# Performance work log

Measured on AMD Instinct MI355X. Metric: run time of the kernel, lower is better.

Reference implementation:

```python
import jax, jax.numpy as jnp
import numpy as np

B, TD, TC = 64, 800, 80
ENC, H, MA, MO = 128, 400, 10, 20
OUT = MO * 6 + 1  # 121


def _lstm(x, h0, c0, Wih, Whh, bih, bhh):
    # x: (B,T,I); PyTorch gate order i,f,g,o
    xg = jnp.einsum('bti,gi->btg', x, Wih) + (bih + bhh)  # (B,T,4H)
    def step(carry, xg_t):
        h, c = carry
        g = xg_t + h @ Whh.T
        i, f, gg, o = jnp.split(g, 4, axis=-1)
        c = jax.nn.sigmoid(f) * c + jax.nn.sigmoid(i) * jnp.tanh(gg)
        h = jax.nn.sigmoid(o) * jnp.tanh(c)
        return (h, c), h
    (_, _), hs = jax.lax.scan(step, (h0, c0), xg.transpose(1, 0, 2))
    return hs.transpose(1, 0, 2)  # (B,T,H)


def setup_inputs() -> dict:
    key = jax.random.key(0)
    ks = jax.random.split(key, 16)
    s = 0.05
    rn = lambda k, sh, sc=1.0: jax.random.normal(k, sh, jnp.float32) * sc
    I1 = 3 + ENC + H
    return {
        'strokes': rn(ks[0], (B, TD, 3)),
        'context': rn(ks[1], (B, TC, ENC)),
        'context_mask': jnp.ones((B, TC), jnp.float32),
        'h_0': rn(ks[2], (3, 2 * H), s),
        'Wih0': rn(ks[3], (4 * H, 3), s), 'Whh0': rn(ks[4], (4 * H, H), s),
        'bih0': jnp.zeros((4 * H,), jnp.float32), 'bhh0': jnp.zeros((4 * H,), jnp.float32),
        'Wih1': rn(ks[5], (4 * H, I1), s), 'Whh1': rn(ks[6], (4 * H, H), s),
        'bih1': jnp.zeros((4 * H,), jnp.float32), 'bhh1': jnp.zeros((4 * H,), jnp.float32),
        'Wih2': rn(ks[7], (4 * H, I1), s), 'Whh2': rn(ks[8], (4 * H, H), s),
        'bih2': jnp.zeros((4 * H,), jnp.float32), 'bhh2': jnp.zeros((4 * H,), jnp.float32),
        'attn_W': rn(ks[9], (3 * MA, H), s), 'attn_b': jnp.zeros((3 * MA,), jnp.float32),
        'out_W': rn(ks[10], (OUT, 3 * H), s), 'out_b': jnp.zeros((OUT,), jnp.float32),
    }


def reference(strokes, context, context_mask, h_0,
              Wih0, Whh0, bih0, bhh0,
              Wih1, Whh1, bih1, bhh1,
              Wih2, Whh2, bih2, bhh2,
              attn_W, attn_b, out_W, out_b):
    bsz = strokes.shape[0]
    # initial states: h_0[l] split into (h, c)
    init = [(jnp.broadcast_to(h_0[l, :H], (bsz, H)), jnp.broadcast_to(h_0[l, H:], (bsz, H))) for l in range(3)]

    h0s = _lstm(strokes, init[0][0], init[0][1], Wih0, Whh0, bih0, bhh0)  # (B,TD,H)

    # Gaussian monotonic attention
    p = jnp.exp(h0s @ attn_W.T + attn_b)  # (B,TD,3MA)
    alpha, beta, kappa = jnp.split(p, 3, axis=-1)
    kappa = jnp.cumsum(0.2 * kappa, axis=1)  # (B,TD,MA)
    u = jnp.arange(TC, dtype=jnp.float32)  # (TC,)
    # phi: (B,TD,TC)
    diff = kappa[:, :, None, :] - u[None, None, :, None]
    phi = jnp.sum(alpha[:, :, None, :] * jnp.exp(-beta[:, :, None, :] * diff * diff), axis=-1)
    w = jnp.einsum('btu,bue->bte', phi * context_mask[:, None, :], context)  # (B,TD,ENC)

    x1 = jnp.concatenate([strokes, h0s, w], axis=2)
    h1s = _lstm(x1, init[1][0], init[1][1], Wih1, Whh1, bih1, bhh1)
    x2 = jnp.concatenate([strokes, h1s, w], axis=2)
    h2s = _lstm(x2, init[2][0], init[2][1], Wih2, Whh2, bih2, bhh2)

    outputs = jnp.concatenate([h0s, h1s, h2s], axis=-1) @ out_W.T + out_b  # (B,TD,121)
    return outputs
```

## Files before the change

### kernel.cpp

```cpp
#include <hip/hip_runtime.h>
#include <stdint.h>

typedef unsigned short u16;
typedef __attribute__((ext_vector_type(8))) short bf16x8;
typedef __attribute__((ext_vector_type(4))) float f32x4;
typedef __attribute__((ext_vector_type(4))) int   i32x4;
typedef __attribute__((ext_vector_type(4))) unsigned short u16x4;

#define DI static __device__ __forceinline__

constexpr int B_   = 64;
constexpr int TD   = 800;
constexpr int TC   = 80;
constexpr int ENC  = 128;
constexpr int H    = 400;
constexpr int OUTN = 121;

constexpr int HP   = 416;
constexpr int KT_H = 13;
constexpr int KOP  = 1216;
constexpr int NOP  = 128;
constexpr int NBL  = 25;
constexpr int NBA  = 32;
constexpr int CSTR = 32;
constexpr int FSLOT= 32;

constexpr size_t HB_B  = (size_t)(TD+1)*B_*HP*2;
constexpr size_t WBF_B = (size_t)TD*B_*ENC*2;
constexpr size_t STR_B = (size_t)TD*B_*4*4;
constexpr size_t APK_B = (size_t)NBL*4*KT_H*64*8*2;
constexpr size_t WF_B  = (size_t)NBL*4*17*64*8*2;

constexpr size_t OFF_HB0 = 0;
constexpr size_t OFF_HB1 = OFF_HB0 + HB_B;
constexpr size_t OFF_HB2 = OFF_HB1 + HB_B;
constexpr size_t OFF_HLO = OFF_HB2 + HB_B;
constexpr size_t OFF_WBF = OFF_HLO + HB_B;
constexpr size_t OFF_STR = OFF_WBF + WBF_B;
constexpr size_t OFF_APKH= OFF_STR + STR_B;
constexpr size_t OFF_APKL= OFF_APKH + 3*APK_B;
constexpr size_t OFF_WF1 = OFF_APKL + APK_B;
constexpr size_t OFF_WF2 = OFF_WF1 + WF_B;
constexpr size_t OFF_OUW = OFF_WF2 + WF_B;
constexpr size_t OFF_BIA = OFF_OUW + (size_t)NOP*KOP*2;
constexpr size_t OFF_CNT = OFF_BIA + (size_t)3*1600*4;
constexpr size_t WS_NEED = OFF_CNT + (size_t)4*FSLOT*CSTR*4 + 256;

constexpr int LDS_DUMP = 0;
constexpr int LDS_CL   = 66560;
constexpr int LDS_EX   = 70656;
constexpr int LDS_W3   = 140288;
constexpr int LDS_BIAS = 141056;
constexpr int LDSB     = 141312;
constexpr int ALDS_CTX = 0;
constexpr int ALDS_ATW = 81920;
constexpr int ALDS_H   = 130040;
constexpr int ALDS_PHI = 133240;
constexpr int ALDS_MSK = 133880;
constexpr int ALDS_KAP = 134520;
constexpr int ALDS_P   = 134600;
constexpr int ALDS_PPS = 134840;

DI u16 f2b(float f){ union{float f; unsigned u;} v; v.f=f; unsigned r = v.u + 0x7FFFu + ((v.u>>16)&1u); return (u16)(r>>16); }
DI float b2f(u16 h){ union{unsigned u; float f;} v; v.u=((unsigned)h)<<16; return v.f; }
DI float sigm(float x){ return 1.f/(1.f+__expf(-x)); }
DI float tanh_(float x){ float a=fabsf(x), e=__expf(-2.f*a), t=(1.f-e)/(1.f+e); return x<0.f ? -t : t; }

DI void st16(u16* p, u16 v){
  asm volatile("global_store_short %0, %1, off sc0 sc1" :: "v"(p), "v"((unsigned)v) : "memory");
}
DI void st8(u16* p, u16x4 v){
  unsigned long long x; __builtin_memcpy(&x, &v, 8);
  asm volatile("global_store_dwordx2 %0, %1, off sc0 sc1" :: "v"(p), "v"(x) : "memory");
}
DI void setflag(unsigned* p, unsigned t){
  asm volatile("global_store_dword %0, %1, off sc0 sc1" :: "v"(p), "v"(t) : "memory");
}
DI void waitflags2(const unsigned* fA, int nA, unsigned tA,
                   const unsigned* fB, int nB, unsigned tB){
  int lane = threadIdx.x & 63;
  const unsigned* p; unsigned tgt;
  if (lane < nA)            { p = fA + (size_t)lane*CSTR;        tgt = tA; }
  else if (lane < nA+nB)    { p = fB + (size_t)(lane-nA)*CSTR;   tgt = tB; }
  else                      { p = fA;                            tgt = 0;  }
  while (1) {
    unsigned v = __hip_atomic_load(p, __ATOMIC_RELAXED, __HIP_MEMORY_SCOPE_AGENT);
    if (__all(v >= tgt)) break;
    __builtin_amdgcn_s_sleep(1);
  }
  asm volatile("" ::: "memory");
}

__global__ void k_init(const float* __restrict__ h0, u16* hb0, u16* hb1, u16* hb2, u16* hlo,
                       unsigned* cnt){
  int i = blockIdx.x*256 + threadIdx.x;
  const int nA = 3*B_*HP, nA2 = B_*HP, nB = 4*TD*B_*16, nC = 4*FSLOT;
  if (i < nA) {
    int l = i/(B_*HP); int rem = i - l*(B_*HP); int b = rem/HP; int k = rem - b*HP;
    u16 v = (k<H) ? f2b(h0[l*800 + k]) : (u16)0;
    (l==0?hb0:(l==1?hb1:hb2))[(size_t)b*HP + k] = v;
  } else if (i < nA+nA2) {
    int rem = i - nA; int b = rem/HP; int k = rem - b*HP;
    u16 v = 0;
    if (k < H) { float w = h0[k]; u16 hi = f2b(w); v = f2b(w - b2f(hi)); }
    hlo[(size_t)b*HP + k] = v;
  } else if (i < nA+nA2+nB) {
    int q = i - nA - nA2; int buf = q/(TD*B_*16); int r2 = q % (TD*B_*16);
    int t = r2/(B_*16) + 1; int r3 = r2 % (B_*16); int b = r3>>4; int kk = r3&15;
    u16* hb = (buf==0)?hb0:((buf==1)?hb1:((buf==2)?hb2:hlo));
    hb[((size_t)t*B_ + b)*HP + 400 + kk] = 0;
  } else if (i < nA+nA2+nB+nC) {
    int q = i - nA - nA2 - nB;
    cnt[(size_t)q*CSTR] = 0u;
  }
}

__global__ void k_apack(const float* W0, const float* W1, const float* W2,
                        u16* apkHi, u16* apkLo){
  int i = blockIdx.x*256 + threadIdx.x;
  const int total = 3*NBL*4*KT_H*64;
  if (i >= total) return;
  int lane = i & 63; int r = i >> 6;
  int kt = r % KT_H; r /= KT_H;
  int mt = r % 4;    r /= 4;
  int j  = r % NBL;  int lv = r / NBL;
  const float* W = (lv==0)?W0:((lv==1)?W1:W2);
  int row = mt*400 + j*16 + (lane & 15);
  int kbase = kt*32 + (lane>>4)*8;
  #pragma unroll
  for (int e=0;e<8;++e){
    int k = kbase+e;
    float w = (k<H) ? W[(size_t)row*H + k] : 0.f;
    u16 hi = f2b(w);
    apkHi[(size_t)i*8 + e] = hi;
    if (lv == 0) apkLo[(size_t)i*8 + e] = f2b(w - b2f(hi));
  }
}

__global__ void k_wihpack2(const float* __restrict__ W, u16* __restrict__ dst){
  int i = blockIdx.x*256 + threadIdx.x;
  if (i >= NBL*4*17*64) return;
  int lane = i & 63; int r = i >> 6;
  int ktf = r % 17; r /= 17; int mt = r % 4; int j = r / 4;
  int row = mt*400 + j*16 + (lane & 15);
  int kbase = ktf*32 + (lane>>4)*8;
  #pragma unroll
  for (int e=0;e<8;++e){
    int k = kbase+e;
    int col;
    if (ktf < 13) col = (k < 400) ? (3 + k) : -1;
    else          col = 403 + (k - 416);
    dst[(size_t)i*8 + e] = (col >= 0) ? f2b(W[(size_t)row*531 + col]) : (u16)0;
  }
}

__global__ void k_smallpack(const float* outW,
                            const float* bi0, const float* bh0, const float* bi1, const float* bh1,
                            const float* bi2, const float* bh2,
                            u16* ouw, float* biasP){
  int i = blockIdx.x*256 + threadIdx.x;
  const int n2 = NOP*KOP, n3 = 3*1600;
  if (i < n2) {
    int n = i/KOP, k = i - n*KOP;
    ouw[i] = (n<OUTN && k<1200) ? f2b(outW[(size_t)n*1200 + k]) : (u16)0;
  } else if (i < n2+n3) {
    int q = i-n2; int l = q/1600, row = q - l*1600;
    const float* bi = (l==0)?bi0:((l==1)?bi1:bi2);
    const float* bh = (l==0)?bh0:((l==1)?bh1:bh2);
    biasP[q] = bi[row] + bh[row];
  }
}

__global__ void k_packs(const float* __restrict__ strokes, float* __restrict__ st){
  int i = blockIdx.x*256 + threadIdx.x;
  if (i >= TD*B_) return;
  int t = i / B_, b = i & 63;
  st[(size_t)i*4+0] = strokes[((size_t)b*TD + t)*3 + 0];
  st[(size_t)i*4+1] = strokes[((size_t)b*TD + t)*3 + 1];
  st[(size_t)i*4+2] = strokes[((size_t)b*TD + t)*3 + 2];
  st[(size_t)i*4+3] = 0.f;
}

template<int L>
DI void stage_lstm(char* smem, int j,
    const u16* __restrict__ apkHi,
    const u16* __restrict__ exG,
    const float* __restrict__ strokesT,
    const float* __restrict__ wihRaw, int wihStride,
    const float* __restrict__ biasL,
    const float* __restrict__ h0g,
    u16* __restrict__ hb_self, const u16* __restrict__ hb_prev,
    u16* __restrict__ hlo_, const u16* __restrict__ wbf,
    unsigned* __restrict__ fSelf, const unsigned* __restrict__ fDep, int nDep)
{
  float* dumpS = (float*)(smem + LDS_DUMP);
  float* cL    = (float*)(smem + LDS_CL);
  u16*   exS   = (u16*)  (smem + LDS_EX);
  float* w3S   = (float*)(smem + LDS_W3);
  float* biasS = (float*)(smem + LDS_BIAS);
  const int tid = threadIdx.x, wv = tid>>6, l = tid&63;
  const int col = l&15, kg = l>>4;

  bf16x8 ahi[4][4];
  #pragma unroll
  for (int mt=0;mt<4;++mt)
    #pragma unroll
    for (int i=0;i<4;++i){
      int kt = wv + i*4;
      if (kt < KT_H) ahi[mt][i] = *(const bf16x8*)(apkHi + (size_t)j*26624 + ((size_t)(mt*KT_H + kt)*64 + l)*8);
      else { bf16x8 z = {0,0,0,0,0,0,0,0}; ahi[mt][i] = z; }
    }
  {
    const int nv = (L==0) ? 3328 : 4352;
    const size_t stride = (L==0) ? 26624 : 34816;
    const i32x4* src = (const i32x4*)(exG + (size_t)j*stride);
    i32x4* dst = (i32x4*)exS;
    for (int i = tid; i < nv; i += 256) dst[i] = src[i];
  }
  if (tid < 192) {
    int local = tid/3, c = tid - (tid/3)*3;
    int row = (local>>4)*400 + j*16 + (local&15);
    w3S[tid] = wihRaw[(size_t)row*wihStride + c];
  }
  if (tid < 64) {
    int row = (tid>>4)*400 + j*16 + (tid&15);
    biasS[tid] = biasL[row];
  }
  for (int i = tid; i < 1024; i += 256) cL[i] = h0g[L*800 + 400 + j*16 + (i>>6)];
  __syncthreads();

  for (int t = 1; t <= TD; ++t) {
    if constexpr (L > 0) waitflags2(fDep, nDep, (unsigned)t, fSelf, NBL, (unsigned)(t-1));
    else                 waitflags2(fSelf, NBL, (unsigned)(t-1), nullptr, 0, 0u);
    f32x4 acc[4][4];
    #pragma unroll
    for (int mt=0;mt<4;++mt)
      #pragma unroll
      for (int nt=0;nt<4;++nt){ f32x4 z = {0.f,0.f,0.f,0.f}; acc[mt][nt] = z; }

    const u16* hbase = hb_self + (size_t)(t-1)*B_*HP + kg*8;
    const u16* lbase = (L==0) ? (hlo_ + (size_t)(t-1)*B_*HP + kg*8) : nullptr;
    #pragma unroll
    for (int i=0;i<4;++i){
      int kt = wv + i*4;
      if (kt < KT_H) {
        bf16x8 bhi[4], blo[4];
        #pragma unroll
        for (int nt=0;nt<4;++nt){
          bhi[nt] = *(const bf16x8*)(hbase + (size_t)(nt*16+col)*HP + kt*32);
          if constexpr (L==0) blo[nt] = *(const bf16x8*)(lbase + (size_t)(nt*16+col)*HP + kt*32);
        }
        #pragma unroll
        for (int mt=0;mt<4;++mt){
          bf16x8 a = ahi[mt][i];
          #pragma unroll
          for (int nt=0;nt<4;++nt)
            acc[mt][nt] = __builtin_amdgcn_mfma_f32_16x16x32_bf16(a, bhi[nt], acc[mt][nt], 0,0,0);
          if constexpr (L==0) {
            bf16x8 al = *(const bf16x8*)(exS + ((size_t)(mt*KT_H + kt)*64 + l)*8);
            #pragma unroll
            for (int nt=0;nt<4;++nt){
              acc[mt][nt] = __builtin_amdgcn_mfma_f32_16x16x32_bf16(a,  blo[nt], acc[mt][nt], 0,0,0);
              acc[mt][nt] = __builtin_amdgcn_mfma_f32_16x16x32_bf16(al, bhi[nt], acc[mt][nt], 0,0,0);
            }
          }
        }
      }
    }
    if constexpr (L > 0) {
      const u16* pbase = hb_prev + (size_t)t*B_*HP + kg*8;
      const u16* wbase = wbf + ((size_t)(t-1)*B_)*ENC + kg*8;
      #pragma unroll
      for (int i=0;i<5;++i){
        int ktf = wv + i*4;
        if (ktf < 17) {
          bf16x8 bfr[4];
          if (ktf < 13) {
            #pragma unroll
            for (int nt=0;nt<4;++nt) bfr[nt] = *(const bf16x8*)(pbase + (size_t)(nt*16+col)*HP + ktf*32);
          } else {
            #pragma unroll
            for (int nt=0;nt<4;++nt) bfr[nt] = *(const bf16x8*)(wbase + (size_t)(nt*16+col)*ENC + (ktf-13)*32);
          }
          #pragma unroll
          for (int mt=0;mt<4;++mt){
            bf16x8 a = *(const bf16x8*)(exS + ((size_t)(mt*17 + ktf)*64 + l)*8);
            #pragma unroll
            for (int nt=0;nt<4;++nt)
              acc[mt][nt] = __builtin_amdgcn_mfma_f32_16x16x32_bf16(a, bfr[nt], acc[mt][nt], 0,0,0);
          }
        }
      }
    }
    #pragma unroll
    for (int mt=0;mt<4;++mt)
      #pragma unroll
      for (int nt=0;nt<4;++nt)
        #pragma unroll
        for (int r=0;r<4;++r)
          dumpS[wv*4160 + (mt*16 + kg*4 + r)*65 + nt*16 + col] = acc[mt][nt][r];
    __syncthreads();
    {
      const int bg = tid & 63, uq = tid >> 6;
      const float* sp = strokesT + ((size_t)(t-1)*B_ + bg)*4;
      float sx = sp[0], sy = sp[1], sz = sp[2];
      u16x4 hh4, ll4;
      #pragma unroll
      for (int e=0;e<4;++e){
        int u = uq*4 + e;
        int idx = u*64 + bg;
        float gv[4];
        #pragma unroll
        for (int g=0; g<4; ++g){
          int row = g*16 + u;
          float s = dumpS[row*65 + bg] + dumpS[4160 + row*65 + bg]
                  + dumpS[8320 + row*65 + bg] + dumpS[12480 + row*65 + bg];
          s += biasS[row] + w3S[row*3+0]*sx + w3S[row*3+1]*sy + w3S[row*3+2]*sz;
          gv[g] = s;
        }
        float co = cL[idx];
        float i_ = sigm(gv[0]), f_ = sigm(gv[1]), g_ = tanh_(gv[2]), o_ = sigm(gv[3]);
        float cn = f_*co + i_*g_;
        cL[idx] = cn;
        float hv = o_*tanh_(cn);
        u16 hh = f2b(hv);
        hh4[e] = hh;
        if constexpr (L==0) ll4[e] = f2b(hv - b2f(hh));
      }
      st8(hb_self + ((size_t)t*B_ + bg)*HP + j*16 + uq*4, hh4);
      if constexpr (L==0) st8(hlo_ + ((size_t)t*B_ + bg)*HP + j*16 + uq*4, ll4);
    }
    __syncthreads();
    if (tid == 0) setflag(fSelf + (size_t)j*CSTR, (unsigned)t);
  }
}

DI void stage_attn(char* smem, int j2,
    const float* __restrict__ ctx, const float* __restrict__ cmask,
    const float* __restrict__ attnW, const float* __restrict__ attnB,
    const u16* __restrict__ hb0, const u16* __restrict__ hlo_,
    u16* __restrict__ wbf,
    const unsigned* __restrict__ fA, unsigned* __restrict__ fB)
{
  float* ctxS = (float*)(smem + ALDS_CTX);
  float* atwS = (float*)(smem + ALDS_ATW);
  float* hS   = (float*)(smem + ALDS_H);
  float* phiS = (float*)(smem + ALDS_PHI);
  float* mskS = (float*)(smem + ALDS_MSK);
  float* kapS = (float*)(smem + ALDS_KAP);
  float* pS   = (float*)(smem + ALDS_P);
  float* ppsS = (float*)(smem + ALDS_PPS);
  const int tid = threadIdx.x;
  const int b0 = j2*2;
  for (int i = tid; i < 2*80*128; i += 256) {
    int bi = i/10240, rem = i%10240;
    ctxS[i] = ctx[(size_t)(b0+bi)*10240 + rem];
  }
  for (int i = tid; i < 30*400; i += 256) {
    int row = i/400, k = i - row*400;
    atwS[row*401 + k] = attnW[i];
  }
  for (int i = tid; i < 160; i += 256) {
    int bi = i/80, u = i - bi*80;
    mskS[i] = cmask[(b0+bi)*80 + u];
  }
  if (tid < 20) kapS[tid] = 0.f;
  float aB = (tid < 60) ? attnB[tid % 30] : 0.f;
  __syncthreads();

  for (int t = 1; t <= TD; ++t) {
    waitflags2(fA, NBL, (unsigned)t, nullptr, 0, 0u);
    if (tid < 200) {
      int bi = tid/100, k = (tid%100)*4;
      size_t off = ((size_t)t*B_ + (b0+bi))*HP + k;
      u16x4 hi4 = *(const u16x4*)(hb0 + off);
      u16x4 lo4 = *(const u16x4*)(hlo_ + off);
      #pragma unroll
      for (int e=0;e<4;++e) hS[bi*400 + k + e] = b2f(hi4[e]) + b2f(lo4[e]);
    }
    __syncthreads();
    if (tid < 240) {
      int bi = tid/120, r = tid - bi*120;
      int row = r>>2, seg = r&3;
      const float* ar = atwS + row*401 + seg*100;
      const float* hr = hS + bi*400 + seg*100;
      float a0=0,a1=0,a2=0,a3=0;
      #pragma unroll 4
      for (int k=0;k<100;k+=4){
        a0 += ar[k]*hr[k]; a1 += ar[k+1]*hr[k+1];
        a2 += ar[k+2]*hr[k+2]; a3 += ar[k+3]*hr[k+3];
      }
      ppsS[(bi*30+row)*4+seg] = a0+a1+a2+a3;
    }
    __syncthreads();
    if (tid < 60) {
      int bi = tid/30, row = tid - bi*30;
      const float* pp = ppsS + (bi*30+row)*4;
      pS[bi*30+row] = __expf(pp[0]+pp[1]+pp[2]+pp[3] + aB);
    }
    __syncthreads();
    if (tid < 20) {
      int bi = tid/10, m = tid - bi*10;
      kapS[tid] += 0.2f * pS[bi*30 + 20 + m];
    }
    __syncthreads();
    if (tid < 160) {
      int bi = tid/80; float u2 = (float)(tid - bi*80);
      const float* pb = pS + bi*30; const float* kb = kapS + bi*10;
      float a = 0.f;
      #pragma unroll
      for (int m=0;m<10;++m){ float d = kb[m]-u2; a += pb[m]*__expf(-pb[10+m]*d*d); }
      phiS[tid] = a * mskS[tid];
    }
    __syncthreads();
    {
      int bi = tid >> 7, e = tid & 127;
      const float* ph = phiS + bi*80;
      const float* cs = ctxS + (size_t)bi*10240 + e;
      float a = 0.f;
      for (int u = 0; u < TC; ++u) a += ph[u]*cs[u*128];
      st16(wbf + ((size_t)(t-1)*B_ + (b0+bi))*ENC + e, f2b(a));
    }
    __syncthreads();
    if (tid == 0) setflag(fB + (size_t)j2*CSTR, (unsigned)t);
  }
}

__global__ __launch_bounds__(256,1) void k_mega(
    const u16* apkH, const u16* apkL, const u16* wf1, const u16* wf2,
    const float* strokesT, const float* Wih0, const float* Wih1, const float* Wih2,
    const float* bia, const float* h0g,
    u16* hb0, u16* hb1, u16* hb2, u16* hlo, u16* wbf,
    const float* ctx, const float* cmask, const float* attnW, const float* attnB,
    unsigned* cnt)
{
  extern __shared__ char smem[];
  unsigned* fA = cnt;
  unsigned* fB = cnt + (size_t)FSLOT*CSTR;
  unsigned* fC = cnt + (size_t)2*FSLOT*CSTR;
  unsigned* fD = cnt + (size_t)3*FSLOT*CSTR;
  int j = blockIdx.x;
  if (j < NBL) {
    stage_lstm<0>(smem, j, apkH, apkL, strokesT, Wih0, 3, bia, h0g,
                  hb0, nullptr, hlo, nullptr, fA, nullptr, 0);
  } else if (j < NBL+NBA) {
    stage_attn(smem, j-NBL, ctx, cmask, attnW, attnB, hb0, hlo, wbf, fA, fB);
  } else if (j < 2*NBL+NBA) {
    stage_lstm<1>(smem, j-NBL-NBA, apkH + (size_t)1*NBL*26624, wf1, strokesT, Wih1, 531,
                  bia+1600, h0g, hb1, hb0, nullptr, wbf, fC, fB, NBA);
  } else {
    stage_lstm<2>(smem, j-2*NBL-NBA, apkH + (size_t)2*NBL*26624, wf2, strokesT, Wih2, 531,
                  bia+3200, h0g, hb2, hb1, nullptr, wbf, fD, fC, NBL);
  }
}

__global__ __launch_bounds__(256) void k_gemm_out(const u16* __restrict__ hb0, const u16* __restrict__ hb1,
                                                  const u16* __restrict__ hb2, const u16* __restrict__ ouw,
                                                  const float* __restrict__ out_b, float* __restrict__ dout){
  int wv = threadIdx.x>>6, l = threadIdx.x&63;
  int task = blockIdx.x*4 + wv;
  int ng = task & 1; int mpair = task >> 1;
  int m0 = mpair*32; int t = m0>>6; int broff = m0 & 63;
  int col = l&15, kg = l>>4;
  f32x4 acc[2][4];
  #pragma unroll
  for (int mt=0;mt<2;++mt)
    #pragma unroll
    for (int nt=0;nt<4;++nt){ f32x4 z = {0.f,0.f,0.f,0.f}; acc[mt][nt] = z; }
  for (int kt=0; kt<38; ++kt) {
    int k0 = kt*32 + kg*8;
    int reg = (k0>=800) ? 2 : ((k0>=400) ? 1 : 0);
    int koff = k0 - reg*400;
    const u16* hb = (reg==0) ? hb0 : ((reg==1) ? hb1 : hb2);
    bf16x8 afr[2];
    #pragma unroll
    for (int mt=0;mt<2;++mt)
      afr[mt] = *(const bf16x8*)(hb + ((size_t)(t+1)*B_ + broff + mt*16 + col)*HP + koff);
    #pragma unroll
    for (int nt=0;nt<4;++nt) {
      bf16x8 bfr = *(const bf16x8*)(ouw + (size_t)(ng*64 + nt*16 + col)*KOP + k0);
      #pragma unroll
      for (int mt=0;mt<2;++mt)
        acc[mt][nt] = __builtin_amdgcn_mfma_f32_16x16x32_bf16(afr[mt], bfr, acc[mt][nt], 0,0,0);
    }
  }
  #pragma unroll
  for (int mt=0;mt<2;++mt)
    #pragma unroll
    for (int nt=0;nt<4;++nt)
      #pragma unroll
      for (int r=0;r<4;++r) {
        int n = ng*64 + nt*16 + col;
        int bo = broff + mt*16 + kg*4 + r;
        if (n < OUTN) dout[((size_t)bo*TD + t)*OUTN + n] = acc[mt][nt][r] + out_b[n];
      }
}

__global__ void k_sentinel(float* o, float code){ o[threadIdx.x] = code; }

extern "C" void kernel_launch(void* const* d_in, const int* in_sizes, int n_in,
                              void* d_out, int out_size, void* d_ws, size_t ws_size,
                              hipStream_t stream) {
  const float* strokes = (const float*)d_in[0];
  const float* context = (const float*)d_in[1];
  const float* cmask   = (const float*)d_in[2];
  const float* h0      = (const float*)d_in[3];
  const float* Wih0 = (const float*)d_in[4];  const float* Whh0 = (const float*)d_in[5];
  const float* bih0 = (const float*)d_in[6];  const float* bhh0 = (const float*)d_in[7];
  const float* Wih1 = (const float*)d_in[8];  const float* Whh1 = (const float*)d_in[9];
  const float* bih1 = (const float*)d_in[10]; const float* bhh1 = (const float*)d_in[11];
  const float* Wih2 = (const float*)d_in[12]; const float* Whh2 = (const float*)d_in[13];
  const float* bih2 = (const float*)d_in[14]; const float* bhh2 = (const float*)d_in[15];
  const float* attnW = (const float*)d_in[16]; const float* attnB = (const float*)d_in[17];
  const float* outW  = (const float*)d_in[18]; const float* outB  = (const float*)d_in[19];
  float* dout = (float*)d_out;

  if (ws_size < WS_NEED) {
    float code = 1000.0f + (float)(ws_size >> 20);
    k_sentinel<<<1, 64, 0, stream>>>(dout, code);
    return;
  }

  char* ws = (char*)d_ws;
  u16* hb0 = (u16*)(ws + OFF_HB0);
  u16* hb1 = (u16*)(ws + OFF_HB1);
  u16* hb2 = (u16*)(ws + OFF_HB2);
  u16* hlo = (u16*)(ws + OFF_HLO);
  u16* wbf = (u16*)(ws + OFF_WBF);
  float* strT = (float*)(ws + OFF_STR);
  u16* apkH = (u16*)(ws + OFF_APKH);
  u16* apkL = (u16*)(ws + OFF_APKL);
  u16* wf1  = (u16*)(ws + OFF_WF1);
  u16* wf2  = (u16*)(ws + OFF_WF2);
  u16* ouw  = (u16*)(ws + OFF_OUW);
  float* bia = (float*)(ws + OFF_BIA);
  unsigned* cnt = (unsigned*)(ws + OFF_CNT);

  (void)hipFuncSetAttribute((const void*)k_mega, hipFuncAttributeMaxDynamicSharedMemorySize, LDSB);

  {
    int n = 3*B_*HP + B_*HP + 4*TD*B_*16 + 4*FSLOT;
    k_init<<<(n+255)/256, 256, 0, stream>>>(h0, hb0, hb1, hb2, hlo, cnt);
  }
  k_apack<<<(3*NBL*4*KT_H*64+255)/256, 256, 0, stream>>>(Whh0, Whh1, Whh2, apkH, apkL);
  k_wihpack2<<<(NBL*4*17*64+255)/256, 256, 0, stream>>>(Wih1, wf1);
  k_wihpack2<<<(NBL*4*17*64+255)/256, 256, 0, stream>>>(Wih2, wf2);
  {
    int n = NOP*KOP + 3*1600;
    k_smallpack<<<(n+255)/256, 256, 0, stream>>>(outW, bih0,bhh0,bih1,bhh1,bih2,bhh2, ouw, bia);
  }
  k_packs<<<(TD*B_+255)/256, 256, 0, stream>>>(strokes, strT);

  k_mega<<<2*NBL+NBA+NBL, 256, LDSB, stream>>>(apkH, apkL, wf1, wf2,
      strT, Wih0, Wih1, Wih2, bia, h0,
      hb0, hb1, hb2, hlo, wbf,
      context, cmask, attnW, attnB, cnt);

  k_gemm_out<<<3200/4, 256, 0, stream>>>(hb0, hb1, hb2, ouw, outB, dout);
}
```

Baseline: 7.855 ms.

## Place each LSTM stage on one XCC and exchange recurrent state through XCC-local buffers

The persistent kernel is launched as 256 blocks, and block indices are mapped to stages with stride 8 so that each LSTM layer's 25 blocks are expected to land on the same XCC. A runtime check reads HW_REG_XCC_ID and confirms this. If it holds, the recurrent hidden state and the step flags are exchanged through small double-buffered volatile buffers instead of system-coherent stores and atomics. Flag polling is also limited to one wave per block, followed by a barrier. This targets the cost of cross-die coherence on the per-timestep dependency chain. It relies on the hardware's block-to-XCC placement, and plain volatile loads inside one XCC's L2 could be subtle to get right for correctness.

```diff
diff --git a/kernel.cpp b/kernel.cpp
--- a/kernel.cpp
+++ b/kernel.cpp
@@ -30,6 +30,7 @@
 constexpr size_t STR_B = (size_t)TD*B_*4*4;
 constexpr size_t APK_B = (size_t)NBL*4*KT_H*64*8*2;
 constexpr size_t WF_B  = (size_t)NBL*4*17*64*8*2;
+constexpr size_t LOC_B = (size_t)2*B_*HP*2;
 
 constexpr size_t OFF_HB0 = 0;
 constexpr size_t OFF_HB1 = OFF_HB0 + HB_B;
@@ -44,14 +45,21 @@
 constexpr size_t OFF_OUW = OFF_WF2 + WF_B;
 constexpr size_t OFF_BIA = OFF_OUW + (size_t)NOP*KOP*2;
 constexpr size_t OFF_CNT = OFF_BIA + (size_t)3*1600*4;
-constexpr size_t WS_NEED = OFF_CNT + (size_t)4*FSLOT*CSTR*4 + 256;
+constexpr size_t OFF_XCC = OFF_CNT + (size_t)4*FSLOT*CSTR*4;
+constexpr size_t OFF_FLG = OFF_XCC + (size_t)3*FSLOT*CSTR*4;
+constexpr size_t OFF_HL0 = OFF_FLG + (size_t)3*FSLOT*CSTR*4;
+constexpr size_t OFF_LL0 = OFF_HL0 + LOC_B;
+constexpr size_t OFF_HL1 = OFF_LL0 + LOC_B;
+constexpr size_t OFF_HL2 = OFF_HL1 + LOC_B;
+constexpr size_t WS_NEED = OFF_HL2 + LOC_B + 256;
 
 constexpr int LDS_DUMP = 0;
 constexpr int LDS_CL   = 66560;
 constexpr int LDS_EX   = 70656;
 constexpr int LDS_W3   = 140288;
 constexpr int LDS_BIAS = 141056;
-constexpr int LDSB     = 141312;
+constexpr int LDS_VERD = 141312;
+constexpr int LDSB     = 141568;
 constexpr int ALDS_CTX = 0;
 constexpr int ALDS_ATW = 81920;
 constexpr int ALDS_H   = 130040;
@@ -90,11 +98,30 @@
   }
   asm volatile("" ::: "memory");
 }
+DI void waitloc(const unsigned* f, int n, unsigned tgt){
+  int lane = threadIdx.x & 63;
+  const volatile unsigned* p = (const volatile unsigned*)(f + (size_t)((lane<n)?lane:0)*CSTR);
+  while (1) {
+    unsigned v = *p;
+    if (__all(v >= tgt)) break;
+    __builtin_amdgcn_s_sleep(1);
+  }
+  asm volatile("" ::: "memory");
+}
+DI bf16x8 vld8(const u16* p){
+  i32x4 v = *(const volatile i32x4*)p;
+  bf16x8 r; __builtin_memcpy(&r, &v, 16); return r;
+}
+DI int get_xcc(){
+  int x; asm volatile("s_getreg_b32 %0, hwreg(HW_REG_XCC_ID)" : "=s"(x)); return x & 0xff;
+}
 
 __global__ void k_init(const float* __restrict__ h0, u16* hb0, u16* hb1, u16* hb2, u16* hlo,
-                       unsigned* cnt){
+                       unsigned* cnt, unsigned* xccb, unsigned* flgb,
+                       u16* hl0, u16* ll0, u16* hl1, u16* hl2){
   int i = blockIdx.x*256 + threadIdx.x;
-  const int nA = 3*B_*HP, nA2 = B_*HP, nB = 4*TD*B_*16, nC = 4*FSLOT;
+  const int nA = 3*B_*HP, nA2 = B_*HP, nB = 4*TD*B_*16, nC = 4*FSLOT, nD = 6*FSLOT;
+  const int nE = 4*2*B_*HP;
   if (i < nA) {
     int l = i/(B_*HP); int rem = i - l*(B_*HP); int b = rem/HP; int k = rem - b*HP;
     u16 v = (k<H) ? f2b(h0[l*800 + k]) : (u16)0;
@@ -112,6 +139,22 @@
   } else if (i < nA+nA2+nB+nC) {
     int q = i - nA - nA2 - nB;
     cnt[(size_t)q*CSTR] = 0u;
+  } else if (i < nA+nA2+nB+nC+nD) {
+    int q = i - nA - nA2 - nB - nC;
+    if (q < 3*FSLOT) xccb[(size_t)q*CSTR] = 0u;
+    else             flgb[(size_t)(q-3*FSLOT)*CSTR] = 0u;
+  } else if (i < nA+nA2+nB+nC+nD+nE) {
+    int q = i - nA - nA2 - nB - nC - nD;
+    int buf = q / (2*B_*HP); int rem = q % (2*B_*HP);
+    int k = rem % HP;
+    u16 v = 0;
+    if (k < H) {
+      if (buf == 0)      v = f2b(h0[k]);
+      else if (buf == 1) { float w = h0[k]; u16 hi = f2b(w); v = f2b(w - b2f(hi)); }
+      else if (buf == 2) v = f2b(h0[800 + k]);
+      else               v = f2b(h0[1600 + k]);
+    }
+    (buf==0?hl0:(buf==1?ll0:(buf==2?hl1:hl2)))[rem] = v;
   }
 }
 
@@ -181,17 +224,16 @@
   st[(size_t)i*4+3] = 0.f;
 }
 
-template<int L>
+template<int L, bool LOC>
 DI void stage_lstm(char* smem, int j,
-    const u16* __restrict__ apkHi,
-    const u16* __restrict__ exG,
+    const u16* __restrict__ apkHi, const u16* __restrict__ exG,
     const float* __restrict__ strokesT,
     const float* __restrict__ wihRaw, int wihStride,
-    const float* __restrict__ biasL,
-    const float* __restrict__ h0g,
+    const float* __restrict__ biasL, const float* __restrict__ h0g,
     u16* __restrict__ hb_self, const u16* __restrict__ hb_prev,
     u16* __restrict__ hlo_, const u16* __restrict__ wbf,
-    unsigned* __restrict__ fSelf, const unsigned* __restrict__ fDep, int nDep)
+    unsigned* __restrict__ fSelf, const unsigned* __restrict__ fDep, int nDep,
+    u16* __restrict__ hloc, u16* __restrict__ lloc, unsigned* __restrict__ flgS)
 {
   float* dumpS = (float*)(smem + LDS_DUMP);
   float* cL    = (float*)(smem + LDS_CL);
@@ -230,16 +272,26 @@
   __syncthreads();
 
   for (int t = 1; t <= TD; ++t) {
-    if constexpr (L > 0) waitflags2(fDep, nDep, (unsigned)t, fSelf, NBL, (unsigned)(t-1));
-    else                 waitflags2(fSelf, NBL, (unsigned)(t-1), nullptr, 0, 0u);
+    if (wv == 0) {
+      if constexpr (L > 0) waitflags2(fDep, nDep, (unsigned)t, nullptr, 0, 0u);
+      if constexpr (LOC)   waitloc(flgS, NBL, (unsigned)(t-1));
+      else                 waitflags2(fSelf, NBL, (unsigned)(t-1), nullptr, 0, 0u);
+    }
+    __syncthreads();
     f32x4 acc[4][4];
     #pragma unroll
     for (int mt=0;mt<4;++mt)
       #pragma unroll
       for (int nt=0;nt<4;++nt){ f32x4 z = {0.f,0.f,0.f,0.f}; acc[mt][nt] = z; }
 
-    const u16* hbase = hb_self + (size_t)(t-1)*B_*HP + kg*8;
-    const u16* lbase = (L==0) ? (hlo_ + (size_t)(t-1)*B_*HP + kg*8) : nullptr;
+    const u16* hbase; const u16* lbase = nullptr;
+    if constexpr (LOC) {
+      hbase = hloc + (size_t)((t-1)&1)*B_*HP + kg*8;
+      if constexpr (L==0) lbase = lloc + (size_t)((t-1)&1)*B_*HP + kg*8;
+    } else {
+      hbase = hb_self + (size_t)(t-1)*B_*HP + kg*8;
+      if constexpr (L==0) lbase = hlo_ + (size_t)(t-1)*B_*HP + kg*8;
+    }
     #pragma unroll
     for (int i=0;i<4;++i){
       int kt = wv + i*4;
@@ -247,8 +299,12 @@
         bf16x8 bhi[4], blo[4];
         #pragma unroll
         for (int nt=0;nt<4;++nt){
-          bhi[nt] = *(const bf16x8*)(hbase + (size_t)(nt*16+col)*HP + kt*32);
-          if constexpr (L==0) blo[nt] = *(const bf16x8*)(lbase + (size_t)(nt*16+col)*HP + kt*32);
+          if constexpr (LOC) bhi[nt] = vld8(hbase + (size_t)(nt*16+col)*HP + kt*32);
+          else               bhi[nt] = *(const bf16x8*)(hbase + (size_t)(nt*16+col)*HP + kt*32);
+          if constexpr (L==0) {
+            if constexpr (LOC) blo[nt] = vld8(lbase + (size_t)(nt*16+col)*HP + kt*32);
+            else               blo[nt] = *(const bf16x8*)(lbase + (size_t)(nt*16+col)*HP + kt*32);
+          }
         }
         #pragma unroll
         for (int mt=0;mt<4;++mt){
@@ -327,11 +383,18 @@
         hh4[e] = hh;
         if constexpr (L==0) ll4[e] = f2b(hv - b2f(hh));
       }
+      if constexpr (LOC) {
+        *(u16x4*)(hloc + ((size_t)(t&1)*B_ + bg)*HP + j*16 + uq*4) = hh4;
+        if constexpr (L==0) *(u16x4*)(lloc + ((size_t)(t&1)*B_ + bg)*HP + j*16 + uq*4) = ll4;
+      }
       st8(hb_self + ((size_t)t*B_ + bg)*HP + j*16 + uq*4, hh4);
       if constexpr (L==0) st8(hlo_ + ((size_t)t*B_ + bg)*HP + j*16 + uq*4, ll4);
     }
     __syncthreads();
-    if (tid == 0) setflag(fSelf + (size_t)j*CSTR, (unsigned)t);
+    if (tid == 0) {
+      if constexpr (LOC) *((volatile unsigned*)(flgS + (size_t)j*CSTR)) = (unsigned)t;
+      setflag(fSelf + (size_t)j*CSTR, (unsigned)t);
+    }
   }
 }
 
@@ -369,7 +432,8 @@
   __syncthreads();
 
   for (int t = 1; t <= TD; ++t) {
-    waitflags2(fA, NBL, (unsigned)t, nullptr, 0, 0u);
+    if ((tid>>6) == 0) waitflags2(fA, NBL, (unsigned)t, nullptr, 0, 0u);
+    __syncthreads();
     if (tid < 200) {
       int bi = tid/100, k = (tid%100)*4;
       size_t off = ((size_t)t*B_ + (b0+bi))*HP + k;
@@ -426,31 +490,60 @@
   }
 }
 
+DI bool xcc_check(char* smem, int stage, int j, unsigned* xccb){
+  unsigned* xs = xccb + (size_t)stage*FSLOT*CSTR;
+  if (threadIdx.x == 0) setflag(xs + (size_t)j*CSTR, 0x100u | (unsigned)get_xcc());
+  if ((threadIdx.x>>6) == 0) {
+    waitflags2(xs, NBL, 0x100u, nullptr, 0, 0u);
+    int lane = threadIdx.x & 63;
+    unsigned v = __hip_atomic_load(xs + (size_t)((lane<NBL)?lane:0)*CSTR,
+                                   __ATOMIC_RELAXED, __HIP_MEMORY_SCOPE_AGENT);
+    unsigned r0 = __shfl(v, 0);
+    int uni = __all(v == r0) ? 1 : 0;
+    if (threadIdx.x == 0) *(int*)(smem + LDS_VERD) = uni;
+  }
+  __syncthreads();
+  return (*(int*)(smem + LDS_VERD)) != 0;
+}
+
 __global__ __launch_bounds__(256,1) void k_mega(
     const u16* apkH, const u16* apkL, const u16* wf1, const u16* wf2,
     const float* strokesT, const float* Wih0, const float* Wih1, const float* Wih2,
     const float* bia, const float* h0g,
     u16* hb0, u16* hb1, u16* hb2, u16* hlo, u16* wbf,
     const float* ctx, const float* cmask, const float* attnW, const float* attnB,
-    unsigned* cnt)
+    unsigned* cnt, unsigned* xccb, unsigned* flgb,
+    u16* hl0, u16* ll0, u16* hl1, u16* hl2)
 {
   extern __shared__ char smem[];
   unsigned* fA = cnt;
   unsigned* fB = cnt + (size_t)FSLOT*CSTR;
   unsigned* fC = cnt + (size_t)2*FSLOT*CSTR;
   unsigned* fD = cnt + (size_t)3*FSLOT*CSTR;
-  int j = blockIdx.x;
-  if (j < NBL) {
-    stage_lstm<0>(smem, j, apkH, apkL, strokesT, Wih0, 3, bia, h0g,
-                  hb0, nullptr, hlo, nullptr, fA, nullptr, 0);
-  } else if (j < NBL+NBA) {
-    stage_attn(smem, j-NBL, ctx, cmask, attnW, attnB, hb0, hlo, wbf, fA, fB);
-  } else if (j < 2*NBL+NBA) {
-    stage_lstm<1>(smem, j-NBL-NBA, apkH + (size_t)1*NBL*26624, wf1, strokesT, Wih1, 531,
-                  bia+1600, h0g, hb1, hb0, nullptr, wbf, fC, fB, NBA);
-  } else {
-    stage_lstm<2>(smem, j-2*NBL-NBA, apkH + (size_t)2*NBL*26624, wf2, strokesT, Wih2, 531,
-                  bia+3200, h0g, hb2, hb1, nullptr, wbf, fD, fC, NBL);
+  int b = blockIdx.x; int colx = b & 7; int row = b >> 3;
+  if (colx == 0 && row < NBL) {
+    bool loc = xcc_check(smem, 0, row, xccb);
+    if (loc) stage_lstm<0,true >(smem, row, apkH, apkL, strokesT, Wih0, 3, bia, h0g,
+                  hb0, nullptr, hlo, nullptr, fA, nullptr, 0, hl0, ll0, flgb);
+    else     stage_lstm<0,false>(smem, row, apkH, apkL, strokesT, Wih0, 3, bia, h0g,
+                  hb0, nullptr, hlo, nullptr, fA, nullptr, 0, hl0, ll0, flgb);
+  } else if ((colx == 1 || colx == 2) && row < 16) {
+    int j2 = (colx-1)*16 + row;
+    stage_attn(smem, j2, ctx, cmask, attnW, attnB, hb0, hlo, wbf, fA, fB);
+  } else if (colx == 3 && row < NBL) {
+    bool loc = xcc_check(smem, 1, row, xccb);
+    unsigned* fg = flgb + (size_t)FSLOT*CSTR;
+    if (loc) stage_lstm<1,true >(smem, row, apkH + (size_t)1*NBL*26624, wf1, strokesT, Wih1, 531,
+                  bia+1600, h0g, hb1, hb0, nullptr, wbf, fC, fB, NBA, hl1, nullptr, fg);
+    else     stage_lstm<1,false>(smem, row, apkH + (size_t)1*NBL*26624, wf1, strokesT, Wih1, 531,
+                  bia+1600, h0g, hb1, hb0, nullptr, wbf, fC, fB, NBA, hl1, nullptr, fg);
+  } else if (colx == 4 && row < NBL) {
+    bool loc = xcc_check(smem, 2, row, xccb);
+    unsigned* fg = flgb + (size_t)2*FSLOT*CSTR;
+    if (loc) stage_lstm<2,true >(smem, row, apkH + (size_t)2*NBL*26624, wf2, strokesT, Wih2, 531,
+                  bia+3200, h0g, hb2, hb1, nullptr, wbf, fD, fC, NBL, hl2, nullptr, fg);
+    else     stage_lstm<2,false>(smem, row, apkH + (size_t)2*NBL*26624, wf2, strokesT, Wih2, 531,
+                  bia+3200, h0g, hb2, hb1, nullptr, wbf, fD, fC, NBL, hl2, nullptr, fg);
   }
 }
 
@@ -535,12 +628,18 @@
   u16* ouw  = (u16*)(ws + OFF_OUW);
   float* bia = (float*)(ws + OFF_BIA);
   unsigned* cnt = (unsigned*)(ws + OFF_CNT);
+  unsigned* xccb = (unsigned*)(ws + OFF_XCC);
+  unsigned* flgb = (unsigned*)(ws + OFF_FLG);
+  u16* hl0 = (u16*)(ws + OFF_HL0);
+  u16* ll0 = (u16*)(ws + OFF_LL0);
+  u16* hl1 = (u16*)(ws + OFF_HL1);
+  u16* hl2 = (u16*)(ws + OFF_HL2);
 
   (void)hipFuncSetAttribute((const void*)k_mega, hipFuncAttributeMaxDynamicSharedMemorySize, LDSB);
 
   {
-    int n = 3*B_*HP + B_*HP + 4*TD*B_*16 + 4*FSLOT;
-    k_init<<<(n+255)/256, 256, 0, stream>>>(h0, hb0, hb1, hb2, hlo, cnt);
+    int n = 3*B_*HP + B_*HP + 4*TD*B_*16 + 4*FSLOT + 6*FSLOT + 4*2*B_*HP;
+    k_init<<<(n+255)/256, 256, 0, stream>>>(h0, hb0, hb1, hb2, hlo, cnt, xccb, flgb, hl0, ll0, hl1, hl2);
   }
   k_apack<<<(3*NBL*4*KT_H*64+255)/256, 256, 0, stream>>>(Whh0, Whh1, Whh2, apkH, apkL);
   k_wihpack2<<<(NBL*4*17*64+255)/256, 256, 0, stream>>>(Wih1, wf1);
@@ -551,10 +650,10 @@
   }
   k_packs<<<(TD*B_+255)/256, 256, 0, stream>>>(strokes, strT);
 
-  k_mega<<<2*NBL+NBA+NBL, 256, LDSB, stream>>>(apkH, apkL, wf1, wf2,
+  k_mega<<<256, 256, LDSB, stream>>>(apkH, apkL, wf1, wf2,
       strT, Wih0, Wih1, Wih2, bia, h0,
       hb0, hb1, hb2, hlo, wbf,
-      context, cmask, attnW, attnB, cnt);
+      context, cmask, attnW, attnB, cnt, xccb, flgb, hl0, ll0, hl1, hl2);
 
   k_gemm_out<<<3200/4, 256, 0, stream>>>(hb0, hb1, hb2, ouw, outB, dout);
 }
```

Result: faster. 7.307 ms (median of 2 runs) (-7.0%).
